# Kernel tuning notes

Measured on AMD Instinct MI355X. Metric: run time of the kernel, lower is better.

The kernel has to match this reference:

```python
import jax, jax.numpy as jnp
import numpy as np

B, C, H, W = 64, 128, 11, 11
OUT = 16
N_SIM = 5
EPS = 1e-2


def _conv3d(x, w, b):
    # x: [b,ci,D,h,w], w: [co,ci,7,3,3], 'same' padding, ReLU
    y = jax.lax.conv_general_dilated(x, w, (1, 1, 1), [(3, 3), (1, 1), (1, 1)],
                                     dimension_numbers=('NCDHW', 'OIDHW', 'NCDHW'))
    return jax.nn.relu(y + b[None, :, None, None, None])


def _conv2d(x, w, b, dil=1):
    p = dil  # 3x3 kernel, 'same' with dilation
    y = jax.lax.conv_general_dilated(x, w, (1, 1), [(p, p), (p, p)], rhs_dilation=(dil, dil),
                                     dimension_numbers=('NCHW', 'OIHW', 'NCHW'))
    return y + b[None, :, None, None]


def _center(f):  # [b,c,h,w] -> [b,c] (center pixel)
    return f[:, :, f.shape[2] // 2, f.shape[3] // 2]


def _ratio(v):  # compute_ratio_withstep: [b,c] -> [b,1,c,c] band-ratio image
    d = v[:, None, :]
    d = jnp.where(jnp.abs(d) < EPS, EPS, d)
    return (v[:, :, None] / d)[:, None, :, :]


def _cpr(sa3d, w):  # CVT3D_2D_SA: spectral-attention collapse [b,16,D,h,w] -> [b,16,h,w]
    a = jax.nn.softmax(w, axis=-1)
    return jax.nn.relu(jnp.einsum('bodhw,od->bohw', sa3d, a))


def _sideout(f2d, w, b):  # sideout2d: mlp on center pixel features
    return _center(f2d) @ w.T + b


def _similar_sum(x, feat, n=N_SIM):
    # topk(n, largest=False) over |feat - center|, gather those pixels from x, sum them
    b, c = x.shape[0], x.shape[1]
    cv = _center(feat).reshape(b, 1, 1, 1)
    diff = jnp.abs(feat - cv).reshape(b, -1)          # [b, h*w]
    _, idx = jax.lax.top_k(-diff, n)                   # n smallest -> [b, n]
    img = x.reshape(b, c, -1)                          # [b, c, h*w]
    idx_b = jnp.broadcast_to(idx[:, None, :], (b, c, n))
    sim = jnp.take_along_axis(img, idx_b, axis=2)      # [b, c, n]
    return sim.sum(axis=2)                             # masked sum over n similar pixels


def _forward(x, w3d1, b3d1, w3d23, b3d23, cpr_w, w2d45, b2d45, seg_w, seg_b,
             so_w, so_b, sp_wa, sp_ba, sp_wb, sp_bb, sp_sw, sp_sb, fuse_para):
    sp_ct = _ratio(_center(x))                         # [b,1,c,c]
    sa1 = _conv3d(x[:, None], w3d1, b3d1)              # [b,16,C,11,11]
    sa1_2d = _cpr(sa1, cpr_w[0])
    sa2 = _conv3d(sa1, w3d23[0], b3d23[0])
    sa2_2d = _cpr(sa2, cpr_w[1])
    sa3 = _conv3d(sa2, w3d23[1], b3d23[1])
    sa3_2d = _cpr(sa3, cpr_w[2])
    sa4_2d = jax.nn.relu(_conv2d(sa3_2d, w2d45[0], b2d45[0]))
    sa5_2d = jax.nn.relu(_conv2d(sa4_2d, w2d45[1], b2d45[1]))

    feats = [sa1_2d, sa2_2d, sa3_2d, sa4_2d, sa5_2d]
    sa_sides, sp_sides = [], []
    for i, f in enumerate(feats):  # fixed 5 structurally-distinct stages
        sa_sides.append(_sideout(f, so_w[i], so_b[i]))
        act = _conv2d(f, seg_w[i], seg_b[i])           # Seg_Conv: [b,1,11,11]
        s = _similar_sum(x, act)                       # [b,C]
        img = jnp.concatenate([_ratio(s), sp_ct], 1)   # [b,2,C,C]
        y = jax.nn.relu(_conv2d(img, sp_wa[i], sp_ba[i], dil=1))
        y = jax.nn.relu(_conv2d(y, sp_wb[i], sp_bb[i], dil=2))
        sp_sides.append(_sideout(y, sp_sw[i], sp_sb[i]))

    sides = sa_sides + sp_sides
    total = sides[0] * fuse_para[0]
    for i in range(1, 10):
        total = total + fuse_para[i] * sides[i]
    return total                                       # [b, OUT]


def setup_inputs() -> dict:
    key = jax.random.key(0)
    ks = jax.random.split(key, 20)
    s = 0.05
    return {
        'x': jax.random.normal(ks[0], (B, C, H, W), jnp.float32),
        'w3d1': jax.random.normal(ks[1], (16, 1, 7, 3, 3), jnp.float32) * s,
        'b3d1': jnp.zeros((16,), jnp.float32),
        'w3d23': jax.random.normal(ks[2], (2, 16, 16, 7, 3, 3), jnp.float32) * s,
        'b3d23': jnp.zeros((2, 16), jnp.float32),
        'cpr_w': jax.random.normal(ks[3], (3, 16, C), jnp.float32) * s,
        'w2d45': jax.random.normal(ks[4], (2, 16, 16, 3, 3), jnp.float32) * s,
        'b2d45': jnp.zeros((2, 16), jnp.float32),
        'seg_w': jax.random.normal(ks[5], (5, 1, 16, 3, 3), jnp.float32) * s,
        'seg_b': jnp.zeros((5, 1), jnp.float32),
        'so_w': jax.random.normal(ks[6], (5, OUT, 16), jnp.float32) * s,
        'so_b': jnp.zeros((5, OUT), jnp.float32),
        'sp_wa': jax.random.normal(ks[7], (5, 16, 2, 3, 3), jnp.float32) * s,
        'sp_ba': jnp.zeros((5, 16), jnp.float32),
        'sp_wb': jax.random.normal(ks[8], (5, 16, 16, 3, 3), jnp.float32) * s,
        'sp_bb': jnp.zeros((5, 16), jnp.float32),
        'sp_sw': jax.random.normal(ks[9], (5, OUT, 16), jnp.float32) * s,
        'sp_sb': jnp.zeros((5, OUT), jnp.float32),
        'fuse_para': jnp.ones((15,), jnp.float32),
    }


def reference(x, w3d1, b3d1, w3d23, b3d23, cpr_w, w2d45, b2d45, seg_w, seg_b,
              so_w, so_b, sp_wa, sp_ba, sp_wb, sp_bb, sp_sw, sp_sb, fuse_para):
    return _forward(x, w3d1, b3d1, w3d23, b3d23, cpr_w, w2d45, b2d45, seg_w, seg_b,
                    so_w, so_b, sp_wa, sp_ba, sp_wb, sp_bb, sp_sw, sp_sb, fuse_para)
```

## Files before the change

### kernel.cpp

```cpp
#include <hip/hip_runtime.h>
#include <hip/hip_bf16.h>


#define F_SLICE (64 * 16 * 121)
#define PKE (64 * 121 * 134 * 16)
#define LHALF 18304
#define AREP_CV 36864

typedef _Float16 half8 __attribute__((ext_vector_type(8)));
typedef float float4v __attribute__((ext_vector_type(4)));
typedef unsigned short u16x8 __attribute__((ext_vector_type(8)));
typedef unsigned short u16x4 __attribute__((ext_vector_type(4)));

typedef __attribute__((address_space(1))) unsigned int gu32;
typedef __attribute__((address_space(3))) unsigned int lu32;

union HU { _Float16 h; unsigned short u; };

__global__ __launch_bounds__(256) void prep_kernel(
    const float* __restrict__ x, const float* __restrict__ cpr_w,
    const float* __restrict__ w3d1, const float* __restrict__ w2d45,
    const float* __restrict__ w3d23, float* __restrict__ x_t,
    float* __restrict__ a_sm, float* __restrict__ wrep1,
    float* __restrict__ wrep2d, unsigned short* __restrict__ arep) {
  const int bx = blockIdx.x, t = threadIdx.x;
  if (bx < 64) {
    __shared__ float tile[128][123];
    const int b = bx;
    const float* xb = x + (size_t)b * 128 * 121;
    for (int idx = t; idx < 128 * 121; idx += 256) {
      int c = idx / 121, p = idx - c * 121;
      tile[c][p] = xb[idx];
    }
    __syncthreads();
    float* ob = x_t + (size_t)b * 121 * 128;
    for (int idx = t; idx < 121 * 128; idx += 256) {
      int p = idx >> 7, c = idx & 127;
      ob[idx] = tile[c][p];
    }
  } else if (bx < 112) {
    __shared__ float red[128];
    const int row = bx - 64;
    float v = (t < 128) ? cpr_w[row * 128 + t] : -3.0e38f;
    if (t < 128) red[t] = v;
    __syncthreads();
    for (int s = 64; s; s >>= 1) {
      if (t < s) red[t] = fmaxf(red[t], red[t + s]);
      __syncthreads();
    }
    float m = red[0];
    __syncthreads();
    float e = (t < 128) ? expf(v - m) : 0.f;
    if (t < 128) red[t] = e;
    __syncthreads();
    for (int s = 64; s; s >>= 1) {
      if (t < s) red[t] += red[t + s];
      __syncthreads();
    }
    if (t < 128) a_sm[row * 128 + t] = e / red[0];
  } else if (bx < 134) {
    int r = (bx - 112) * 256 + t;
    if (r < 1008) {
      int j = r;
      int kw = j % 3; j /= 3;
      int o = j % 8; j /= 8;
      int kh = j % 3; j /= 3;
      int kd = j % 7; j /= 7;
      int gg = j;
      wrep1[r] = w3d1[(gg * 8 + o) * 63 + kd * 9 + kh * 3 + kw];
    } else if (r < 1008 + 4608) {
      int r2 = r - 1008;
      int o = r2 & 15;
      int uv = (r2 >> 4) % 9;
      int ic = (r2 / 144) % 16;
      int layer = r2 / 2304;
      wrep2d[r2] = w2d45[((layer * 16 + o) * 16 + ic) * 9 + uv];
    }
  } else {
    int idx = (bx - 134) * 256 + t;
    if (idx < 2 * AREP_CV) {
      int j = idx & 7;
      int lane = (idx >> 3) & 63;
      int part = (idx >> 9) & 1;
      int rem = idx >> 10;
      int chunk = rem % 36;
      int cv = rem / 36;
      int kw = chunk % 3;
      int grp = chunk / 3;
      int kdp = grp & 3;
      int kh = grp >> 2;
      int m = lane & 15, q = lane >> 4;
      int kd = 2 * kdp + (q >> 1);
      int ic = (q & 1) * 8 + j;
      float w = 0.f;
      if (kd < 7)
        w = w3d23[((cv * 16 + m) * 16 + ic) * 63 + kd * 9 + kh * 3 + kw] *
            256.f;
      _Float16 hi = (_Float16)w;
      HU out;
      out.h = (part == 0) ? hi : (_Float16)(w - (float)hi);
      arep[idx] = out.u;
    }
  }
}

__global__ __launch_bounds__(256, 4) void conv1_kernel(
    const float* __restrict__ in, const float* __restrict__ wrep,
    const float* __restrict__ bias, const float* __restrict__ al,
    unsigned short* __restrict__ pk_hi, unsigned short* __restrict__ pk_lo,
    float* __restrict__ f_out) {
  __shared__ float in_lds[18][134];
  __shared__ float red[2][16][4];
  const int t = threadIdx.x;
  const int bx = blockIdx.x;
  const int b = blockIdx.y;
  const int h = bx / 3;
  const int w0 = (bx % 3) * 4;
  const int lane = t & 63;
  const int wv = t >> 6;
  const int dh = wv & 1;
  const int dd = lane + (dh << 6);
  const int g = __builtin_amdgcn_readfirstlane(wv >> 1);
  const int oc_base = g << 3;

  float acc[8][4];
#pragma unroll
  for (int o = 0; o < 8; ++o)
#pragma unroll
    for (int c = 0; c < 4; ++c) acc[o][c] = 0.f;

  const int ds = t & 127;
  const int half = t >> 7;

  for (int r = half; r < 18; r += 2) {
    int hr = r / 6;
    int wc = r - hr * 6;
    int hh = h - 1 + hr;
    int ww = w0 - 1 + wc;
    bool ok = (hh >= 0) & (hh < 11) & (ww >= 0) & (ww < 11);
    const float* src = in + (((size_t)b) * 121 + hh * 11 + ww) * 128;
    float v = 0.f;
    if (ok && ds >= 3) v = src[ds - 3];
    in_lds[r][ds] = v;
    if (ds < 6) {
      float v2 = 0.f;
      if (ok && ds < 3) v2 = src[125 + ds];
      in_lds[r][128 + ds] = v2;
    }
  }
  __syncthreads();
  const float* wbase = wrep + g * 504;
#pragma unroll
  for (int kd = 0; kd < 7; ++kd) {
#pragma unroll
    for (int kh = 0; kh < 3; ++kh) {
      float ws[24];
      const float* wp = wbase + kd * 72 + kh * 24;
#pragma unroll
      for (int j = 0; j < 24; ++j) ws[j] = wp[j];
      float v[6];
#pragma unroll
      for (int qq = 0; qq < 6; ++qq) v[qq] = in_lds[kh * 6 + qq][dd + kd];
#pragma unroll
      for (int o = 0; o < 8; ++o)
#pragma unroll
        for (int kw = 0; kw < 3; ++kw) {
          float wv_ = ws[o * 3 + kw];
#pragma unroll
          for (int c = 0; c < 4; ++c)
            acc[o][c] = fmaf(wv_, v[kw + c], acc[o][c]);
        }
    }
  }

  const int p0 = h * 11 + w0;
#pragma unroll
  for (int o = 0; o < 8; ++o) {
    float bv = bias[oc_base + o];
#pragma unroll
    for (int c = 0; c < 4; ++c) acc[o][c] = fmaxf(acc[o][c] + bv, 0.f);
  }
#pragma unroll
  for (int c = 0; c < 4; ++c) {
    if (w0 + c < 11) {
      u16x8 hi8, lo8;
#pragma unroll
      for (int o = 0; o < 8; ++o) {
        float s = acc[o][c] * 256.f;
        _Float16 hh = (_Float16)s;
        HU a, bb;
        a.h = hh;
        bb.h = (_Float16)(s - (float)hh);
        hi8[o] = a.u;
        lo8[o] = bb.u;
      }
      size_t base = (((size_t)b * 121 + p0 + c) * 134 + dd + 3) * 16 + oc_base;
      *(u16x8*)&pk_hi[base] = hi8;
      *(u16x8*)&pk_lo[base] = lo8;
    }
  }
  if (dd < 3) {
    u16x8 z = {0, 0, 0, 0, 0, 0, 0, 0};
#pragma unroll
    for (int c = 0; c < 4; ++c) {
      if (w0 + c < 11) {
        size_t b0 = (((size_t)b * 121 + p0 + c) * 134 + dd) * 16 + oc_base;
        size_t b1 =
            (((size_t)b * 121 + p0 + c) * 134 + 131 + dd) * 16 + oc_base;
        *(u16x8*)&pk_hi[b0] = z;
        *(u16x8*)&pk_lo[b0] = z;
        *(u16x8*)&pk_hi[b1] = z;
        *(u16x8*)&pk_lo[b1] = z;
      }
    }
  }
  float alv[8];
#pragma unroll
  for (int o = 0; o < 8; ++o) alv[o] = al[(oc_base + o) * 128 + dd];
#pragma unroll
  for (int o = 0; o < 8; ++o) {
#pragma unroll
    for (int c = 0; c < 4; ++c) {
      float pv = acc[o][c] * alv[o];
#pragma unroll
      for (int off = 32; off; off >>= 1) pv += __shfl_down(pv, off, 64);
      if (lane == 0) red[dh][oc_base + o][c] = pv;
    }
  }
  __syncthreads();
  if (t < 64) {
    int oc = t >> 2, c = t & 3;
    if (w0 + c < 11)
      f_out[((size_t)b * 16 + oc) * 121 + p0 + c] =
          fmaxf(red[0][oc][c] + red[1][oc][c], 0.f);
  }
}

template <bool WRITE_PK>
__global__ __launch_bounds__(512, 2) void conv_mfma_kernel(
    const unsigned short* __restrict__ pin_hi,
    const unsigned short* __restrict__ pin_lo,
    const unsigned short* __restrict__ arep, const float* __restrict__ bias,
    const float* __restrict__ al, unsigned short* __restrict__ pout_hi,
    unsigned short* __restrict__ pout_lo, float* __restrict__ fpart) {
  __shared__ _Float16 lds[2 * LHALF];
  const int t = threadIdx.x;
  const int bx = blockIdx.x, d16 = blockIdx.y, b = blockIdx.z;
  const int lane = t & 63, wave = t >> 6;
  const int n = lane & 15, q = lane >> 4;
  const int hs = wave >> 2, wg = wave & 3;
  const int h = 2 * bx + hs;

#pragma unroll
  for (int i = 0; i < 9; ++i) {
    int u = t + i * 512;
    int lbo = __builtin_amdgcn_readfirstlane((wave << 6) + i * 512);
    if (u < 4576) {
      int part = (u >= 2288) ? 1 : 0;
      int qq = u - part * 2288;
      int pc = qq / 22;
      int dloc = qq - pc * 22;
      int panel = pc >> 1, icq = pc & 1;
      int rr = panel / 13, cc = panel - rr * 13;
      int hh = 2 * bx + rr - 1, ww = cc - 1;
      bool ok = (hh >= 0) & (hh < 11) & (ww >= 0) & (ww < 11);
      if (ok) {
        const unsigned short* srcp = part ? pin_lo : pin_hi;
        const unsigned short* g =
            &srcp[(((size_t)b * 121 + hh * 11 + ww) * 134 + d16 * 16 + dloc) *
                      16 +
                  icq * 8];
        __builtin_amdgcn_global_load_lds((const gu32*)g,
                                         (lu32*)&lds[(size_t)lbo * 8], 16, 0,
                                         0);
      } else {
        u16x8 z = {0, 0, 0, 0, 0, 0, 0, 0};
        *(u16x8*)&lds[(size_t)u * 8] = z;
      }
    }
  }
  float bias_r[4], alr[4];
#pragma unroll
  for (int r = 0; r < 4; ++r) {
    bias_r[r] = bias[q * 4 + r];
    alr[r] = al[(q * 4 + r) * 128 + d16 * 16 + n];
  }
  __syncthreads();

  const int wl0 = wg * 3;
  int cb[5], cbk[5];
  const int base_qn = (q & 1) * 176 + n * 8 + hs * 4576;
  const int kdh = (lane & 32) ? 8 : 0;
#pragma unroll
  for (int j = 0; j < 5; ++j) {
    int colj = wl0 + j;
    if (colj > 12) colj = 12;
    cb[j] = base_qn + colj * 352;
    cbk[j] = cb[j] + kdh;
  }

  float4v acc[3];
#pragma unroll
  for (int tt = 0; tt < 3; ++tt) acc[tt] = (float4v){0.f, 0.f, 0.f, 0.f};

#pragma unroll
  for (int kh = 0; kh < 3; ++kh) {
#pragma unroll
    for (int kdp = 0; kdp < 4; ++kdp) {
      half8 whi[5], wlo[5];
#pragma unroll
      for (int j = 0; j < 5; ++j) {
        int a = ((kdp < 3) ? cbk[j] : cb[j]) + kh * 4576 + kdp * 16;
        whi[j] = *(const half8*)&lds[a];
        wlo[j] = *(const half8*)&lds[a + LHALF];
      }
#pragma unroll
      for (int kw = 0; kw < 3; ++kw) {
        const int c2 = (kh * 4 + kdp) * 3 + kw;
        half8 ahi = *(const half8*)&arep[((c2 * 2 + 0) * 64 + lane) * 8];
        half8 alo = *(const half8*)&arep[((c2 * 2 + 1) * 64 + lane) * 8];
#pragma unroll
        for (int tt = 0; tt < 3; ++tt) {
          const int jj = tt + kw;
          acc[tt] = __builtin_amdgcn_mfma_f32_16x16x32_f16(ahi, whi[jj],
                                                           acc[tt], 0, 0, 0);
          acc[tt] = __builtin_amdgcn_mfma_f32_16x16x32_f16(ahi, wlo[jj],
                                                           acc[tt], 0, 0, 0);
          acc[tt] = __builtin_amdgcn_mfma_f32_16x16x32_f16(alo, whi[jj],
                                                           acc[tt], 0, 0, 0);
        }
      }
    }
  }

#pragma unroll
  for (int tt = 0; tt < 3; ++tt) {
    const int wl = wg * 3 + tt;
    if (h < 11 && wl < 11) {
      const int p = h * 11 + wl;
      float fr[4];
      u16x4 hi4, lo4;
#pragma unroll
      for (int r = 0; r < 4; ++r) {
        float sv = fmaxf(acc[tt][r] * (1.f / 65536.f) + bias_r[r], 0.f);
        fr[r] = sv * alr[r];
        if (WRITE_PK) {
          float s = sv * 256.f;
          _Float16 hh = (_Float16)s;
          HU a, bb;
          a.h = hh;
          bb.h = (_Float16)(s - (float)hh);
          hi4[r] = a.u;
          lo4[r] = bb.u;
        }
      }
      if (WRITE_PK) {
        size_t base =
            (((size_t)b * 121 + p) * 134 + d16 * 16 + n + 3) * 16 + q * 4;
        *(u16x4*)&pout_hi[base] = hi4;
        *(u16x4*)&pout_lo[base] = lo4;
        u16x4 z = {0, 0, 0, 0};
        if (d16 == 0 && n < 3) {
          size_t hb = (((size_t)b * 121 + p) * 134 + n) * 16 + q * 4;
          *(u16x4*)&pout_hi[hb] = z;
          *(u16x4*)&pout_lo[hb] = z;
        }
        if (d16 == 7 && n >= 13) {
          size_t hb = (((size_t)b * 121 + p) * 134 + n + 118) * 16 + q * 4;
          *(u16x4*)&pout_hi[hb] = z;
          *(u16x4*)&pout_lo[hb] = z;
        }
      }
#pragma unroll
      for (int r = 0; r < 4; ++r) {
        float v = fr[r];
        v += __shfl_xor(v, 1, 64);
        v += __shfl_xor(v, 2, 64);
        v += __shfl_xor(v, 4, 64);
        v += __shfl_xor(v, 8, 64);
        if (n == 0)
          fpart[(((size_t)d16 * 64 + b) * 16 + q * 4 + r) * 121 + p] = v;
      }
    }
  }
}

__global__ __launch_bounds__(128) void sp_prep_kernel(
    const float* __restrict__ f1, const float* __restrict__ fpart1,
    const float* __restrict__ fpart2, const float* __restrict__ x_t,
    const float* __restrict__ wrep2d, const float* __restrict__ b2d45,
    const float* __restrict__ seg_w, const float* __restrict__ seg_b,
    const float* __restrict__ so_w, const float* __restrict__ so_b,
    const float* __restrict__ sp_wa, const float* __restrict__ sp_ba,
    const float* __restrict__ sp_wb, const float* __restrict__ sp_bb,
    const float* __restrict__ sp_sw, const float* __restrict__ sp_sb,
    float* __restrict__ sa_sd, float* __restrict__ sp_sd) {
  const int b = blockIdx.x, i = blockIdx.y;
  const int t = threadIdx.x;
  __shared__ float fl[16 * 121];
  __shared__ float buf[16 * 121];
  __shared__ float act[121];
  __shared__ float diffs[121];
  __shared__ int sel[5];
  __shared__ float s7[7], xc7[7];
  __shared__ float P[2][7][7];
  __shared__ float y1[16][9];
  __shared__ float y2[16];

  {
    float* ldst = (i < 3) ? fl : buf;
    if (i == 0) {
      const float* fb = f1 + (size_t)b * 16 * 121;
      for (int idx = t; idx < 16 * 121; idx += 128) ldst[idx] = fb[idx];
    } else {
      const float* fp0 = (i == 1) ? fpart1 : fpart2;
      const size_t boff = (size_t)b * 16 * 121;
      for (int idx = t; idx < 16 * 121; idx += 128) {
        float s = 0.f;
#pragma unroll
        for (int d16 = 0; d16 < 8; ++d16)
          s += fp0[(size_t)d16 * F_SLICE + boff + idx];
        ldst[idx] = fmaxf(s, 0.f);
      }
    }
  }
  __syncthreads();

#define CONV2D_LAYER(SRC, DST, L)                                        \
  if (t < 121) {                                                         \
    int h_ = t / 11, w_ = t - h_ * 11;                                   \
    float a_[16];                                                        \
    _Pragma("unroll") for (int o = 0; o < 16; ++o) a_[o] =               \
        b2d45[(L)*16 + o];                                               \
    for (int ic = 0; ic < 16; ++ic) {                                    \
      _Pragma("unroll") for (int u = 0; u < 3; ++u) {                    \
        int hh_ = h_ + u - 1;                                            \
        _Pragma("unroll") for (int v = 0; v < 3; ++v) {                  \
          int ww_ = w_ + v - 1;                                          \
          float val_ = (hh_ >= 0 && hh_ < 11 && ww_ >= 0 && ww_ < 11)    \
                           ? (SRC)[ic * 121 + hh_ * 11 + ww_]            \
                           : 0.f;                                        \
          const float* wp_ =                                             \
              wrep2d + (((L)*16 + ic) * 9 + u * 3 + v) * 16;             \
          float wr_[16];                                                 \
          _Pragma("unroll") for (int o = 0; o < 16; ++o) wr_[o] = wp_[o];\
          _Pragma("unroll") for (int o = 0; o < 16; ++o) a_[o] =         \
              fmaf(val_, wr_[o], a_[o]);                                 \
        }                                                                \
      }                                                                  \
    }                                                                    \
    _Pragma("unroll") for (int o = 0; o < 16; ++o)(DST)[o * 121 + t] =   \
        fmaxf(a_[o], 0.f);                                               \
  }

  if (i >= 3) {
    CONV2D_LAYER(buf, fl, 0)
    __syncthreads();
    if (i == 4) {
      CONV2D_LAYER(fl, buf, 1)
      __syncthreads();
    }
  }
  const float* F = (i == 4) ? buf : fl;

  if (t < 16) {
    float s = so_b[i * 16 + t];
    const float* swp = so_w + (i * 16 + t) * 16;
    for (int c = 0; c < 16; ++c) s += F[c * 121 + 60] * swp[c];
    sa_sd[((size_t)i * 64 + b) * 16 + t] = s;
  }

  if (t < 121) {
    int h = t / 11, w = t - h * 11;
    float a = seg_b[i];
    const float* sw = seg_w + i * 144;
    for (int ic = 0; ic < 16; ++ic) {
      float w9[9];
#pragma unroll
      for (int j = 0; j < 9; ++j) w9[j] = sw[ic * 9 + j];
#pragma unroll
      for (int u = 0; u < 3; ++u) {
        int hh = h + u - 1;
#pragma unroll
        for (int v = 0; v < 3; ++v) {
          int ww = w + v - 1;
          if (hh >= 0 && hh < 11 && ww >= 0 && ww < 11)
            a = fmaf(F[ic * 121 + hh * 11 + ww], w9[u * 3 + v], a);
        }
      }
    }
    act[t] = a;
  }
  __syncthreads();
  if (t < 121) diffs[t] = fabsf(act[t] - act[60]);
  __syncthreads();

  for (int k = 0; k < 5; ++k) {
    if (t < 64) {
      float d0 = diffs[t];
      int i0 = t;
      float d1 = (t + 64 < 121) ? diffs[t + 64] : 3.0e38f;
      if (d1 < d0) { d0 = d1; i0 = t + 64; }
#pragma unroll
      for (int off = 32; off; off >>= 1) {
        float od = __shfl_down(d0, off, 64);
        int oi = __shfl_down(i0, off, 64);
        if (od < d0 || (od == d0 && oi < i0)) { d0 = od; i0 = oi; }
      }
      if (t == 0) {
        sel[k] = i0;
        diffs[i0] = 3.0e38f;
      }
    }
    __syncthreads();
  }

  if (t < 7) {
    const float* xb = x_t + (size_t)b * 121 * 128;
    float s = 0.f;
    for (int k = 0; k < 5; ++k) s += xb[(size_t)sel[k] * 128 + 61 + t];
    s7[t] = s;
    xc7[t] = xb[60 * 128 + 61 + t];
  }
  __syncthreads();
  if (t < 49) {
    int r = t / 7, c = t - r * 7;
    float d0 = s7[c];
    if (fabsf(d0) < 0.01f) d0 = 0.01f;
    float d1 = xc7[c];
    if (fabsf(d1) < 0.01f) d1 = 0.01f;
    P[0][r][c] = s7[r] / d0;
    P[1][r][c] = xc7[r] / d1;
  }
  __syncthreads();
  for (int item = t; item < 144; item += 128) {
    int ch = item / 9, pos = item - ch * 9;
    int a0 = pos / 3, b0 = pos - a0 * 3;
    float a = sp_ba[i * 16 + ch];
    const float* wa = sp_wa + ((size_t)(i * 16 + ch) * 2) * 9;
#pragma unroll
    for (int icc = 0; icc < 2; ++icc)
#pragma unroll
      for (int u = 0; u < 3; ++u)
#pragma unroll
        for (int v = 0; v < 3; ++v)
          a = fmaf(P[icc][2 * a0 + u][2 * b0 + v], wa[icc * 9 + u * 3 + v], a);
    y1[ch][pos] = fmaxf(a, 0.f);
  }
  __syncthreads();
  if (t < 16) {
    float a = sp_bb[i * 16 + t];
    const float* wb = sp_wb + (size_t)(i * 16 + t) * 16 * 9;
    for (int ch = 0; ch < 16; ++ch)
#pragma unroll
      for (int pos = 0; pos < 9; ++pos)
        a = fmaf(y1[ch][pos], wb[ch * 9 + pos], a);
    y2[t] = fmaxf(a, 0.f);
  }
  __syncthreads();
  if (t < 16) {
    float a = sp_sb[i * 16 + t];
    const float* swp = sp_sw + (size_t)(i * 16 + t) * 16;
    for (int ch = 0; ch < 16; ++ch) a = fmaf(y2[ch], swp[ch], a);
    sp_sd[((size_t)i * 64 + b) * 16 + t] = a;
  }
}

__global__ __launch_bounds__(256) void fuse_kernel(
    const float* __restrict__ sa_sd, const float* __restrict__ sp_sd,
    const float* __restrict__ fp, float* __restrict__ out) {
  int g = blockIdx.x * 256 + threadIdx.x;
  if (g >= 1024) return;
  int b = g >> 4, o = g & 15;
  float tot = 0.f;
  for (int i = 0; i < 5; ++i) {
    tot += fp[i] * sa_sd[((size_t)i * 64 + b) * 16 + o];
    tot += fp[5 + i] * sp_sd[((size_t)i * 64 + b) * 16 + o];
  }
  out[g] = tot;
}

extern "C" void kernel_launch(void* const* d_in, const int* in_sizes, int n_in,
                              void* d_out, int out_size, void* d_ws,
                              size_t ws_size, hipStream_t stream) {
  const float* x = (const float*)d_in[0];
  const float* w3d1 = (const float*)d_in[1];
  const float* b3d1 = (const float*)d_in[2];
  const float* w3d23 = (const float*)d_in[3];
  const float* b3d23 = (const float*)d_in[4];
  const float* cpr_w = (const float*)d_in[5];
  const float* w2d45 = (const float*)d_in[6];
  const float* b2d45 = (const float*)d_in[7];
  const float* seg_w = (const float*)d_in[8];
  const float* seg_b = (const float*)d_in[9];
  const float* so_w = (const float*)d_in[10];
  const float* so_b = (const float*)d_in[11];
  const float* sp_wa = (const float*)d_in[12];
  const float* sp_ba = (const float*)d_in[13];
  const float* sp_wb = (const float*)d_in[14];
  const float* sp_bb = (const float*)d_in[15];
  const float* sp_sw = (const float*)d_in[16];
  const float* sp_sb = (const float*)d_in[17];
  const float* fpar = (const float*)d_in[18];

  float* ws = (float*)d_ws;
  float* x_t = ws;
  float* a_sm = x_t + 991232;
  float* f1 = a_sm + 6144;
  float* fpart1 = f1 + F_SLICE;
  float* fpart2 = fpart1 + 8 * F_SLICE;
  float* sp_sd = fpart2 + 8 * F_SLICE;
  float* sa_sd = sp_sd + 5120;
  float* wrep1 = sa_sd + 5120;
  float* wrep2d = wrep1 + 1024;
  unsigned short* pk1h = (unsigned short*)(wrep2d + 4608);
  unsigned short* pk1l = pk1h + PKE;
  unsigned short* pk2h = pk1l + PKE;
  unsigned short* pk2l = pk2h + PKE;
  unsigned short* arep = pk2l + PKE;

  prep_kernel<<<422, 256, 0, stream>>>(x, cpr_w, w3d1, w2d45, w3d23, x_t,
                                       a_sm, wrep1, wrep2d, arep);

  conv1_kernel<<<dim3(33, 64), 256, 0, stream>>>(x_t, wrep1, b3d1, a_sm, pk1h,
                                                 pk1l, f1);
  conv_mfma_kernel<true><<<dim3(6, 8, 64), 512, 0, stream>>>(
      pk1h, pk1l, arep, b3d23, a_sm + 2048, pk2h, pk2l, fpart1);
  conv_mfma_kernel<false><<<dim3(6, 8, 64), 512, 0, stream>>>(
      pk2h, pk2l, arep + AREP_CV, b3d23 + 16, a_sm + 4096, nullptr, nullptr,
      fpart2);

  sp_prep_kernel<<<dim3(64, 5), 128, 0, stream>>>(
      f1, fpart1, fpart2, x_t, wrep2d, b2d45, seg_w, seg_b, so_w, so_b,
      sp_wa, sp_ba, sp_wb, sp_bb, sp_sw, sp_sb, sa_sd, sp_sd);
  fuse_kernel<<<4, 256, 0, stream>>>(sa_sd, sp_sd, fpar, (float*)d_out);
}
```

Before: 446.4 us.

## Drop x transpose pass and stage hi/lo input halves in sequential LDS phases

```diff
diff --git a/kernel.cpp b/kernel.cpp
--- a/kernel.cpp
+++ b/kernel.cpp
@@ -18,29 +18,14 @@
 union HU { _Float16 h; unsigned short u; };
 
 __global__ __launch_bounds__(256) void prep_kernel(
-    const float* __restrict__ x, const float* __restrict__ cpr_w,
-    const float* __restrict__ w3d1, const float* __restrict__ w2d45,
-    const float* __restrict__ w3d23, float* __restrict__ x_t,
+    const float* __restrict__ cpr_w, const float* __restrict__ w3d1,
+    const float* __restrict__ w2d45, const float* __restrict__ w3d23,
     float* __restrict__ a_sm, float* __restrict__ wrep1,
     float* __restrict__ wrep2d, unsigned short* __restrict__ arep) {
   const int bx = blockIdx.x, t = threadIdx.x;
-  if (bx < 64) {
-    __shared__ float tile[128][123];
-    const int b = bx;
-    const float* xb = x + (size_t)b * 128 * 121;
-    for (int idx = t; idx < 128 * 121; idx += 256) {
-      int c = idx / 121, p = idx - c * 121;
-      tile[c][p] = xb[idx];
-    }
-    __syncthreads();
-    float* ob = x_t + (size_t)b * 121 * 128;
-    for (int idx = t; idx < 121 * 128; idx += 256) {
-      int p = idx >> 7, c = idx & 127;
-      ob[idx] = tile[c][p];
-    }
-  } else if (bx < 112) {
+  if (bx < 48) {
     __shared__ float red[128];
-    const int row = bx - 64;
+    const int row = bx;
     float v = (t < 128) ? cpr_w[row * 128 + t] : -3.0e38f;
     if (t < 128) red[t] = v;
     __syncthreads();
@@ -58,8 +43,8 @@
       __syncthreads();
     }
     if (t < 128) a_sm[row * 128 + t] = e / red[0];
-  } else if (bx < 134) {
-    int r = (bx - 112) * 256 + t;
+  } else if (bx < 70) {
+    int r = (bx - 48) * 256 + t;
     if (r < 1008) {
       int j = r;
       int kw = j % 3; j /= 3;
@@ -77,7 +62,7 @@
       wrep2d[r2] = w2d45[((layer * 16 + o) * 16 + ic) * 9 + uv];
     }
   } else {
-    int idx = (bx - 134) * 256 + t;
+    int idx = (bx - 70) * 256 + t;
     if (idx < 2 * AREP_CV) {
       int j = idx & 7;
       int lane = (idx >> 3) & 63;
@@ -105,7 +90,7 @@
 }
 
 __global__ __launch_bounds__(256, 4) void conv1_kernel(
-    const float* __restrict__ in, const float* __restrict__ wrep,
+    const float* __restrict__ x, const float* __restrict__ wrep,
     const float* __restrict__ bias, const float* __restrict__ al,
     unsigned short* __restrict__ pk_hi, unsigned short* __restrict__ pk_lo,
     float* __restrict__ f_out) {
@@ -138,13 +123,13 @@
     int hh = h - 1 + hr;
     int ww = w0 - 1 + wc;
     bool ok = (hh >= 0) & (hh < 11) & (ww >= 0) & (ww < 11);
-    const float* src = in + (((size_t)b) * 121 + hh * 11 + ww) * 128;
+    const float* src = x + (size_t)b * 15488 + hh * 11 + ww;
     float v = 0.f;
-    if (ok && ds >= 3) v = src[ds - 3];
+    if (ok && ds >= 3) v = src[(ds - 3) * 121];
     in_lds[r][ds] = v;
     if (ds < 6) {
       float v2 = 0.f;
-      if (ok && ds < 3) v2 = src[125 + ds];
+      if (ok && ds < 3) v2 = src[(125 + ds) * 121];
       in_lds[r][128 + ds] = v2;
     }
   }
@@ -243,7 +228,7 @@
     const unsigned short* __restrict__ arep, const float* __restrict__ bias,
     const float* __restrict__ al, unsigned short* __restrict__ pout_hi,
     unsigned short* __restrict__ pout_lo, float* __restrict__ fpart) {
-  __shared__ _Float16 lds[2 * LHALF];
+  __shared__ _Float16 lds[LHALF];
   const int t = threadIdx.x;
   const int bx = blockIdx.x, d16 = blockIdx.y, b = blockIdx.z;
   const int lane = t & 63, wave = t >> 6;
@@ -251,41 +236,33 @@
   const int hs = wave >> 2, wg = wave & 3;
   const int h = 2 * bx + hs;
 
-#pragma unroll
-  for (int i = 0; i < 9; ++i) {
+  int goff[5], loff[5];
+#pragma unroll
+  for (int i = 0; i < 5; ++i) {
     int u = t + i * 512;
-    int lbo = __builtin_amdgcn_readfirstlane((wave << 6) + i * 512);
-    if (u < 4576) {
-      int part = (u >= 2288) ? 1 : 0;
-      int qq = u - part * 2288;
-      int pc = qq / 22;
-      int dloc = qq - pc * 22;
+    if (u < 2288) {
+      int pc = u / 22;
+      int dloc = u - pc * 22;
       int panel = pc >> 1, icq = pc & 1;
       int rr = panel / 13, cc = panel - rr * 13;
       int hh = 2 * bx + rr - 1, ww = cc - 1;
       bool ok = (hh >= 0) & (hh < 11) & (ww >= 0) & (ww < 11);
-      if (ok) {
-        const unsigned short* srcp = part ? pin_lo : pin_hi;
-        const unsigned short* g =
-            &srcp[(((size_t)b * 121 + hh * 11 + ww) * 134 + d16 * 16 + dloc) *
-                      16 +
-                  icq * 8];
-        __builtin_amdgcn_global_load_lds((const gu32*)g,
-                                         (lu32*)&lds[(size_t)lbo * 8], 16, 0,
-                                         0);
-      } else {
-        u16x8 z = {0, 0, 0, 0, 0, 0, 0, 0};
-        *(u16x8*)&lds[(size_t)u * 8] = z;
-      }
-    }
-  }
+      loff[i] = u * 8;
+      goff[i] = ok ? (((b * 121 + hh * 11 + ww) * 134 + d16 * 16 + dloc) * 16 +
+                      icq * 8)
+                   : -1;
+    } else {
+      loff[i] = -1;
+      goff[i] = -1;
+    }
+  }
+
   float bias_r[4], alr[4];
 #pragma unroll
   for (int r = 0; r < 4; ++r) {
     bias_r[r] = bias[q * 4 + r];
     alr[r] = al[(q * 4 + r) * 128 + d16 * 16 + n];
   }
-  __syncthreads();
 
   const int wl0 = wg * 3;
   int cb[5], cbk[5];
@@ -304,15 +281,29 @@
   for (int tt = 0; tt < 3; ++tt) acc[tt] = (float4v){0.f, 0.f, 0.f, 0.f};
 
 #pragma unroll
+  for (int i = 0; i < 5; ++i) {
+    int lbo = __builtin_amdgcn_readfirstlane((wave << 6) + i * 512);
+    if (loff[i] >= 0) {
+      if (goff[i] >= 0) {
+        __builtin_amdgcn_global_load_lds((const gu32*)&pin_hi[goff[i]],
+                                         (lu32*)&lds[(size_t)lbo * 8], 16, 0,
+                                         0);
+      } else {
+        u16x8 z = {0, 0, 0, 0, 0, 0, 0, 0};
+        *(u16x8*)&lds[loff[i]] = z;
+      }
+    }
+  }
+  __syncthreads();
+#pragma unroll
   for (int kh = 0; kh < 3; ++kh) {
 #pragma unroll
     for (int kdp = 0; kdp < 4; ++kdp) {
-      half8 whi[5], wlo[5];
+      half8 wv5[5];
 #pragma unroll
       for (int j = 0; j < 5; ++j) {
         int a = ((kdp < 3) ? cbk[j] : cb[j]) + kh * 4576 + kdp * 16;
-        whi[j] = *(const half8*)&lds[a];
-        wlo[j] = *(const half8*)&lds[a + LHALF];
+        wv5[j] = *(const half8*)&lds[a];
       }
 #pragma unroll
       for (int kw = 0; kw < 3; ++kw) {
@@ -321,14 +312,48 @@
         half8 alo = *(const half8*)&arep[((c2 * 2 + 1) * 64 + lane) * 8];
 #pragma unroll
         for (int tt = 0; tt < 3; ++tt) {
-          const int jj = tt + kw;
-          acc[tt] = __builtin_amdgcn_mfma_f32_16x16x32_f16(ahi, whi[jj],
+          acc[tt] = __builtin_amdgcn_mfma_f32_16x16x32_f16(ahi, wv5[tt + kw],
                                                            acc[tt], 0, 0, 0);
-          acc[tt] = __builtin_amdgcn_mfma_f32_16x16x32_f16(ahi, wlo[jj],
-                                                           acc[tt], 0, 0, 0);
-          acc[tt] = __builtin_amdgcn_mfma_f32_16x16x32_f16(alo, whi[jj],
+          acc[tt] = __builtin_amdgcn_mfma_f32_16x16x32_f16(alo, wv5[tt + kw],
                                                            acc[tt], 0, 0, 0);
         }
+      }
+    }
+  }
+  __syncthreads();
+#pragma unroll
+  for (int i = 0; i < 5; ++i) {
+    int lbo = __builtin_amdgcn_readfirstlane((wave << 6) + i * 512);
+    if (loff[i] >= 0) {
+      if (goff[i] >= 0) {
+        __builtin_amdgcn_global_load_lds((const gu32*)&pin_lo[goff[i]],
+                                         (lu32*)&lds[(size_t)lbo * 8], 16, 0,
+                                         0);
+      } else {
+        u16x8 z = {0, 0, 0, 0, 0, 0, 0, 0};
+        *(u16x8*)&lds[loff[i]] = z;
+      }
+    }
+  }
+  __syncthreads();
+#pragma unroll
+  for (int kh = 0; kh < 3; ++kh) {
+#pragma unroll
+    for (int kdp = 0; kdp < 4; ++kdp) {
+      half8 wv5[5];
+#pragma unroll
+      for (int j = 0; j < 5; ++j) {
+        int a = ((kdp < 3) ? cbk[j] : cb[j]) + kh * 4576 + kdp * 16;
+        wv5[j] = *(const half8*)&lds[a];
+      }
+#pragma unroll
+      for (int kw = 0; kw < 3; ++kw) {
+        const int c2 = (kh * 4 + kdp) * 3 + kw;
+        half8 ahi = *(const half8*)&arep[((c2 * 2 + 0) * 64 + lane) * 8];
+#pragma unroll
+        for (int tt = 0; tt < 3; ++tt)
+          acc[tt] = __builtin_amdgcn_mfma_f32_16x16x32_f16(ahi, wv5[tt + kw],
+                                                           acc[tt], 0, 0, 0);
       }
     }
   }
@@ -387,7 +412,7 @@
 
 __global__ __launch_bounds__(128) void sp_prep_kernel(
     const float* __restrict__ f1, const float* __restrict__ fpart1,
-    const float* __restrict__ fpart2, const float* __restrict__ x_t,
+    const float* __restrict__ fpart2, const float* __restrict__ x,
     const float* __restrict__ wrep2d, const float* __restrict__ b2d45,
     const float* __restrict__ seg_w, const float* __restrict__ seg_b,
     const float* __restrict__ so_w, const float* __restrict__ so_b,
@@ -516,11 +541,11 @@
   }
 
   if (t < 7) {
-    const float* xb = x_t + (size_t)b * 121 * 128;
+    const float* xb = x + (size_t)b * 15488;
     float s = 0.f;
-    for (int k = 0; k < 5; ++k) s += xb[(size_t)sel[k] * 128 + 61 + t];
+    for (int k = 0; k < 5; ++k) s += xb[(61 + t) * 121 + sel[k]];
     s7[t] = s;
-    xc7[t] = xb[60 * 128 + 61 + t];
+    xc7[t] = xb[(61 + t) * 121 + 60];
   }
   __syncthreads();
   if (t < 49) {
@@ -604,8 +629,7 @@
   const float* fpar = (const float*)d_in[18];
 
   float* ws = (float*)d_ws;
-  float* x_t = ws;
-  float* a_sm = x_t + 991232;
+  float* a_sm = ws;
   float* f1 = a_sm + 6144;
   float* fpart1 = f1 + F_SLICE;
   float* fpart2 = fpart1 + 8 * F_SLICE;
@@ -619,10 +643,10 @@
   unsigned short* pk2l = pk2h + PKE;
   unsigned short* arep = pk2l + PKE;
 
-  prep_kernel<<<422, 256, 0, stream>>>(x, cpr_w, w3d1, w2d45, w3d23, x_t,
-                                       a_sm, wrep1, wrep2d, arep);
-
-  conv1_kernel<<<dim3(33, 64), 256, 0, stream>>>(x_t, wrep1, b3d1, a_sm, pk1h,
+  prep_kernel<<<358, 256, 0, stream>>>(cpr_w, w3d1, w2d45, w3d23, a_sm, wrep1,
+                                       wrep2d, arep);
+
+  conv1_kernel<<<dim3(33, 64), 256, 0, stream>>>(x, wrep1, b3d1, a_sm, pk1h,
                                                  pk1l, f1);
   conv_mfma_kernel<true><<<dim3(6, 8, 64), 512, 0, stream>>>(
       pk1h, pk1l, arep, b3d23, a_sm + 2048, pk2h, pk2l, fpart1);
@@ -631,7 +655,7 @@
       fpart2);
 
   sp_prep_kernel<<<dim3(64, 5), 128, 0, stream>>>(
-      f1, fpart1, fpart2, x_t, wrep2d, b2d45, seg_w, seg_b, so_w, so_b,
-      sp_wa, sp_ba, sp_wb, sp_bb, sp_sw, sp_sb, sa_sd, sp_sd);
+      f1, fpart1, fpart2, x, wrep2d, b2d45, seg_w, seg_b, so_w, so_b, sp_wa,
+      sp_ba, sp_wb, sp_bb, sp_sw, sp_sb, sa_sd, sp_sd);
   fuse_kernel<<<4, 256, 0, stream>>>(sa_sd, sp_sd, fpar, (float*)d_out);
 }
```

Result: slower. 547.6 us (+22.7%).
